# Performance work log

Hardware: AMD Instinct MI355X
Metric: run time of the kernel (lower is better)

Reference implementation:

```python
import jax, jax.numpy as jnp
import numpy as np
import math

BASE_RES = 16; SCALE = 1.47; N_LEVELS = 16; FDIM = 2; MAX_SPLASH = 4
LOG2 = 17; HM = 1 << LOG2; SPLITS = [0.9375, 0.875]  # sorted descending as in module


def _build_cfg():
    res = [int(BASE_RES * SCALE ** i) for i in range(N_LEVELS)]
    ns = [0] * N_LEVELS
    for i in range(N_LEVELS):
        for j, s in enumerate(SPLITS):
            if i >= N_LEVELS * s:
                ns[i] = MAX_SPLASH // (2 ** j)
                break
    nidx = [min(r ** 3, HM) for r in res]
    nfeat = [nidx[i] * max(ns[i], 1) for i in range(N_LEVELS)]
    ngau = [nidx[i] * ns[i] for i in range(N_LEVELS)]
    fb = np.concatenate([[0], np.cumsum(nfeat)]).astype(np.int64)
    gb = np.concatenate([[0], np.cumsum(ngau)]).astype(np.int64)
    return res, ns, nidx, fb, gb

RES, NS, NIDX, FB, GB = _build_cfg()
OFFS = np.array([[(k >> 2) & 1, (k >> 1) & 1, k & 1] for k in range(8)], dtype=np.int32)
PRIMES = np.array([1, 2654435761, 805459861], dtype=np.uint32)
SQRT2PI = math.sqrt(2.0 * math.pi)


def _corners_coeffs(coords, res):
    # coords: (N,3) in [0,1). Returns corners (N,8,3) int32 and trilinear coeffs (N,8).
    x = jnp.clip(res * coords, 0.0, res - 1.001)
    pos = jnp.floor(x).astype(jnp.int32)
    xf = x - pos.astype(coords.dtype)
    offs = jnp.asarray(OFFS)
    corners = pos[:, None, :] + offs[None]
    w = jnp.where(offs[None].astype(bool), xf[:, None, :], 1.0 - xf[:, None, :])
    return corners, jnp.prod(w, axis=-1)


def _hash_index(corners, res):
    # linear index if grid fits in table, else xor-prime spatial hash (mod 2^17)
    if res ** 3 <= HM:
        return corners[..., 0] + corners[..., 1] * res + corners[..., 2] * (res * res)
    c = corners.astype(jnp.uint32)
    p = jnp.asarray(PRIMES)
    h = (c[..., 0] * p[0]) ^ (c[..., 1] * p[1]) ^ (c[..., 2] * p[2])
    return (h & jnp.uint32(HM - 1)).astype(jnp.int32)


def setup_inputs() -> dict:
    key = jax.random.key(0)
    k1, k2, k3, k4 = jax.random.split(key, 4)
    N = 262144
    coords = jax.random.uniform(k1, (N, 3), dtype=jnp.float32)
    feats = 0.01 * jax.random.normal(k2, (int(FB[-1]), FDIM), dtype=jnp.float32)
    # means: uniform in a ball of radius 0.25 centered at 0.5 (init_mean)
    G = int(GB[-1])
    pts = jax.random.normal(k3, (G, 3), dtype=jnp.float32)
    r = jnp.sqrt(jax.random.uniform(jax.random.fold_in(k3, 1), (G, 1), dtype=jnp.float32))
    means = pts / jnp.linalg.norm(pts, axis=1, keepdims=True) * r * 0.25 + 0.5
    # stds: N(0.125, 0.02) as in fixed_std=False branch
    stds = 0.125 + 0.02 * jax.random.normal(k4, (G, 1), dtype=jnp.float32)
    return {"coords": coords, "feats": feats, "means": means, "stds": stds}


def reference(coords, feats, means, stds):
    out_feats = []
    out_gmm = []
    for i in range(N_LEVELS):
        res = RES[i]; ns = NS[i]
        corners, coeffs = _corners_coeffs(coords, res)  # (N,8,3), (N,8)
        idx = _hash_index(corners, res)                 # (N,8)
        f = feats[int(FB[i]):int(FB[i + 1])].reshape(-1, max(ns, 1), FDIM)[idx]  # (N,8,S,F)
        if ns:
            m = means[int(GB[i]):int(GB[i + 1])].reshape(-1, ns, 3)[idx]   # (N,8,S,3)
            s = jnp.abs(stds[int(GB[i]):int(GB[i + 1])].reshape(-1, ns, 1)[idx])  # (N,8,S,1)
            diff = coords[:, None, None, :] - m
            sq = jnp.sum(diff * diff / (2.0 * s * s + 1e-7), axis=-1, keepdims=True)
            gw = jnp.exp(-sq) / (SQRT2PI * s + 1e-7)                        # Gaussian weights
            dw = jnp.sum(jnp.abs(diff / s) ** 2, axis=-1, keepdims=True)    # normalized sq dist
            out_feats.append(jnp.einsum('nc,ncsf->nf', coeffs, gw * f))
            out_gmm.append(jnp.einsum('nc,ncs->n', coeffs, (gw * dw)[..., 0]))
        else:
            out_feats.append(jnp.einsum('nc,ncf->nf', coeffs, f[:, :, 0, :]))
    return jnp.concatenate(out_feats, axis=-1), jnp.stack(out_gmm, axis=-1)
```

## Files before the change

kernel.cpp:

```cpp
#include <hip/hip_runtime.h>
#include <math.h>


#define HMASK 131071
typedef float vf4 __attribute__((ext_vector_type(4)));
typedef float vf2 __attribute__((ext_vector_type(2)));
typedef _Float16 h8 __attribute__((ext_vector_type(8)));
typedef unsigned short u16;
typedef unsigned int u32;

#define LIN_OFF 2621440
#define L14_OFF 3670016
#define L15_OFF 7864320

__constant__ int c_fbh[10] = {180567,311639,442711,573783,704855,835927,
                              966999,1098071,1229143,1360215};
__constant__ int c_lres[4] = {16,23,34,50};
__constant__ int c_lfb[4]  = {0,4096,16263,55567};
__constant__ int c_h0res[4] = {74,109,161,237};
__constant__ int c_p1resA[3] = {348,512,753};
__constant__ int c_p1resB[3] = {1108,1629,2394};

__device__ __forceinline__ void corner_setup(int res, float cx, float cy, float cz,
                                             int& px, int& py, int& pz,
                                             float& fx, float& fy, float& fz)
{
    const float hi = (float)res - 1.001f;
    float x = fminf(fmaxf((float)res * cx, 0.0f), hi);
    float y = fminf(fmaxf((float)res * cy, 0.0f), hi);
    float z = fminf(fmaxf((float)res * cz, 0.0f), hi);
    px = (int)x; py = (int)y; pz = (int)z;
    fx = x - (float)px; fy = y - (float)py; fz = z - (float)pz;
}


__device__ __forceinline__ float2 linear_eval4(
    int res, int fbase, float cx, float cy, float cz,
    const float* __restrict__ feats)
{
    int px, py, pz; float fx, fy, fz;
    corner_setup(res, cx, cy, cz, px, py, pz, fx, fy, fz);
    int idxs[4]; float wyz[4];
#pragma unroll
    for (int j = 0; j < 4; ++j) {
        const int oy = (j >> 1) & 1, oz = j & 1;
        idxs[j] = px + (py + oy) * res + (pz + oz) * res * res;
        wyz[j] = (oy ? fy : 1.0f - fy) * (oz ? fz : 1.0f - fz);
    }
    vf4 fv[4];
#pragma unroll
    for (int j = 0; j < 4; ++j)
        fv[j] = *(const vf4*)(feats + (size_t)(fbase + idxs[j]) * 2);
    float a0 = 0.0f, a1 = 0.0f;
    const float gx = 1.0f - fx;
#pragma unroll
    for (int j = 0; j < 4; ++j) {
        a0 += wyz[j] * (gx * fv[j].x + fx * fv[j].z);
        a1 += wyz[j] * (gx * fv[j].y + fx * fv[j].w);
    }
    return make_float2(a0, a1);
}

__device__ __forceinline__ float2 plain_eval_f32h(
    int res, int fbase, float cx, float cy, float cz,
    const float* __restrict__ feats)
{
    int px, py, pz; float fx, fy, fz;
    corner_setup(res, cx, cy, cz, px, py, pz, fx, fy, fz);
    int   idxs[8];
    float ws[8];
#pragma unroll
    for (int k = 0; k < 8; ++k) {
        const int ox = (k >> 2) & 1, oy = (k >> 1) & 1, oz = k & 1;
        const int ix = px + ox, iy = py + oy, iz = pz + oz;
        ws[k] = (ox ? fx : 1.0f - fx) * (oy ? fy : 1.0f - fy) * (oz ? fz : 1.0f - fz);
        unsigned h = (unsigned)ix ^ ((unsigned)iy * 2654435761u) ^ ((unsigned)iz * 805459861u);
        idxs[k] = (int)(h & HMASK);
    }
    float2 fv[8];
#pragma unroll
    for (int k = 0; k < 8; ++k)
        fv[k] = *(const float2*)(feats + (size_t)(fbase + idxs[k]) * 2);
    float a0 = 0.0f, a1 = 0.0f;
#pragma unroll
    for (int k = 0; k < 8; ++k) { a0 += ws[k] * fv[k].x; a1 += ws[k] * fv[k].y; }
    return make_float2(a0, a1);
}


__device__ __forceinline__ float2 linear_eval4_fp8(
    int res, int ebase, float cx, float cy, float cz,
    const u32* __restrict__ ltab)
{
    int px, py, pz; float fx, fy, fz;
    corner_setup(res, cx, cy, cz, px, py, pz, fx, fy, fz);
    int idxs[4]; float wyz[4];
#pragma unroll
    for (int j = 0; j < 4; ++j) {
        const int oy = (j >> 1) & 1, oz = j & 1;
        idxs[j] = px + (py + oy) * res + (pz + oz) * res * res;
        wyz[j] = (oy ? fy : 1.0f - fy) * (oz ? fz : 1.0f - fz);
    }
    u32 u[4];
#pragma unroll
    for (int j = 0; j < 4; ++j) u[j] = ltab[ebase + idxs[j]];
    float a0 = 0.0f, a1 = 0.0f;
    const float gx = 1.0f - fx;
#pragma unroll
    for (int j = 0; j < 4; ++j) {
        vf2 lo = __builtin_amdgcn_cvt_pk_f32_fp8((int)u[j], false);
        vf2 hi = __builtin_amdgcn_cvt_pk_f32_fp8((int)u[j], true);
        a0 += wyz[j] * (gx * lo.x + fx * hi.x);
        a1 += wyz[j] * (gx * lo.y + fx * hi.y);
    }
    return make_float2(a0 * 0.0625f, a1 * 0.0625f);
}

__device__ __forceinline__ float2 plain_eval_fp8(
    int res, const u16* __restrict__ tab, float cx, float cy, float cz)
{
    int px, py, pz; float fx, fy, fz;
    corner_setup(res, cx, cy, cz, px, py, pz, fx, fy, fz);
    int   idxs[8];
    float ws[8];
#pragma unroll
    for (int k = 0; k < 8; ++k) {
        const int ox = (k >> 2) & 1, oy = (k >> 1) & 1, oz = k & 1;
        const int ix = px + ox, iy = py + oy, iz = pz + oz;
        ws[k] = (ox ? fx : 1.0f - fx) * (oy ? fy : 1.0f - fy) * (oz ? fz : 1.0f - fz);
        unsigned h = (unsigned)ix ^ ((unsigned)iy * 2654435761u) ^ ((unsigned)iz * 805459861u);
        idxs[k] = (int)(h & HMASK);
    }
    u16 v[8];
#pragma unroll
    for (int k = 0; k < 8; ++k) v[k] = tab[idxs[k]];
    float a0 = 0.0f, a1 = 0.0f;
#pragma unroll
    for (int k = 0; k < 8; ++k) {
        vf2 d = __builtin_amdgcn_cvt_pk_f32_fp8((int)v[k], false);
        a0 += ws[k] * d.x; a1 += ws[k] * d.y;
    }
    return make_float2(a0 * 0.0625f, a1 * 0.0625f);
}


__device__ __forceinline__ void gauss_pre(float w, float dx, float dy, float dz,
                                          float i2s, float inrm, float is2,
                                          float f0, float f1,
                                          float& a0, float& a1, float& ag)
{
    const float d2 = dx*dx + dy*dy + dz*dz;
    const float sq = d2 * i2s;
    const float gw = __expf(-sq) * inrm;
    const float wg = w * gw;
    a0 += wg * f0;
    a1 += wg * f1;
    ag += wg * (d2 * is2);
}

__device__ __forceinline__ void splash14_part(
    int k0, float cx, float cy, float cz, float cox, float coy, float coz,
    const h8* __restrict__ slots, float& a0, float& a1, float& ag)
{
    int px, py, pz; float fx, fy, fz;
    corner_setup(3520, cx, cy, cz, px, py, pz, fx, fy, fz);
    a0 = 0.0f; a1 = 0.0f; ag = 0.0f;
#pragma unroll
    for (int kk = 0; kk < 2; ++kk) {
        const int k = k0 + kk;
        const int ox = (k >> 2) & 1, oy = (k >> 1) & 1, oz = k & 1;
        const int ix = px + ox, iy = py + oy, iz = pz + oz;
        const float w = (ox ? fx : 1.0f - fx) * (oy ? fy : 1.0f - fy) * (oz ? fz : 1.0f - fz);
        unsigned h = (unsigned)ix ^ ((unsigned)iy * 2654435761u) ^ ((unsigned)iz * 805459861u);
        const int idx = (int)(h & HMASK);
        const h8* sp = slots + (size_t)idx * 2;
        h8 A = sp[0], B = sp[1];
        gauss_pre(w, cox - (float)A[0], coy - (float)A[1], coz - (float)A[2],
                  (float)A[6], (float)B[0], (float)B[2], (float)B[4], (float)B[5], a0, a1, ag);
        gauss_pre(w, cox - (float)A[3], coy - (float)A[4], coz - (float)A[5],
                  (float)A[7], (float)B[1], (float)B[3], (float)B[6], (float)B[7], a0, a1, ag);
    }
}

__device__ __forceinline__ void splash15_part(
    int k, float cx, float cy, float cz, float cox, float coy, float coz,
    const h8* __restrict__ slots, float& a0, float& a1, float& ag)
{
    int px, py, pz; float fx, fy, fz;
    corner_setup(5174, cx, cy, cz, px, py, pz, fx, fy, fz);
    a0 = 0.0f; a1 = 0.0f; ag = 0.0f;
    const int ox = (k >> 2) & 1, oy = (k >> 1) & 1, oz = k & 1;
    const int ix = px + ox, iy = py + oy, iz = pz + oz;
    const float w = (ox ? fx : 1.0f - fx) * (oy ? fy : 1.0f - fy) * (oz ? fz : 1.0f - fz);
    unsigned h = (unsigned)ix ^ ((unsigned)iy * 2654435761u) ^ ((unsigned)iz * 805459861u);
    const int idx = (int)(h & HMASK);
    const h8* sp = slots + (size_t)idx * 4;
    h8 A = sp[0], B = sp[1], C = sp[2], D = sp[3];
    gauss_pre(w, cox - (float)A[0], coy - (float)A[1], coz - (float)A[2],
              (float)B[4], (float)C[0], (float)C[4], (float)D[0], (float)D[1], a0, a1, ag);
    gauss_pre(w, cox - (float)A[3], coy - (float)A[4], coz - (float)A[5],
              (float)B[5], (float)C[1], (float)C[5], (float)D[2], (float)D[3], a0, a1, ag);
    gauss_pre(w, cox - (float)A[6], coy - (float)A[7], coz - (float)B[0],
              (float)B[6], (float)C[2], (float)C[6], (float)D[4], (float)D[5], a0, a1, ag);
    gauss_pre(w, cox - (float)B[1], coy - (float)B[2], coz - (float)B[3],
              (float)B[7], (float)C[3], (float)C[7], (float)D[6], (float)D[7], a0, a1, ag);
}

template<int NS, int KN>
__device__ __forceinline__ void splash_direct_part(
    int k0, int res, int fbase, int gbase, float cx, float cy, float cz,
    const float* __restrict__ feats, const float* __restrict__ means,
    const float* __restrict__ stds, float& a0, float& a1, float& ag)
{
    int px, py, pz; float fx, fy, fz;
    corner_setup(res, cx, cy, cz, px, py, pz, fx, fy, fz);
    a0 = 0.0f; a1 = 0.0f; ag = 0.0f;
#pragma unroll
    for (int kk = 0; kk < KN; ++kk) {
        const int k = k0 + kk;
        const int ox = (k >> 2) & 1, oy = (k >> 1) & 1, oz = k & 1;
        const int ix = px + ox, iy = py + oy, iz = pz + oz;
        const float w = (ox ? fx : 1.0f - fx) * (oy ? fy : 1.0f - fy) * (oz ? fz : 1.0f - fz);
        unsigned h = (unsigned)ix ^ ((unsigned)iy * 2654435761u) ^ ((unsigned)iz * 805459861u);
        const int idx = (int)(h & HMASK);
        const int grow = gbase + idx * NS;
        const float* m = means + (size_t)grow * 3;
        const float* s = stds + grow;
        const float* f = feats + (size_t)(fbase + idx * NS) * 2;
#pragma unroll
        for (int si = 0; si < NS; ++si) {
            const float dx = cx - m[3*si], dy = cy - m[3*si+1], dz = cz - m[3*si+2];
            const float sva = fabsf(s[si]);
            const float d2 = dx*dx + dy*dy + dz*dz;
            const float s2 = sva * sva;
            const float sq = d2 / (2.0f * s2 + 1e-7f);
            const float gw = expf(-sq) / (2.5066282746310002f * sva + 1e-7f);
            const float wg = w * gw;
            a0 += wg * f[2*si];
            a1 += wg * f[2*si+1];
            ag += wg * (d2 / s2);
        }
    }
}

__global__ __launch_bounds__(256) void repack_kernel(
    const float* __restrict__ means, const float* __restrict__ stds,
    const float* __restrict__ feats, unsigned char* __restrict__ wsb)
{
    const int b = blockIdx.x;
    const int tid = threadIdx.x;
    if (b < 640) {
        const int j   = b * 256 + tid;
        const int lvl = j >> 14;
        const int e8  = (j & 16383) * 8;
        const float* src = feats + (size_t)(c_fbh[lvl] + e8) * 2;
        uint4 u;
        u32* up = (u32*)&u;
#pragma unroll
        for (int p = 0; p < 4; ++p) {
            vf4 f = *(const vf4*)(src + 4 * p);
            int w = __builtin_amdgcn_cvt_pk_fp8_f32(16.0f * f.x, 16.0f * f.y, 0, false);
            w = __builtin_amdgcn_cvt_pk_fp8_f32(16.0f * f.z, 16.0f * f.w, w, true);
            up[p] = (u32)w;
        }
        *(uint4*)(wsb + (size_t)lvl * 262144 + (size_t)e8 * 2) = u;
    } else if (b < 1346) {
        const int e = (b - 640) * 256 + tid;
        if (e < 180567) {
            const float2 fa = *(const float2*)(feats + 2 * (size_t)e);
            const float2 fb = *(const float2*)(feats + 2 * (size_t)e + 2);
            int w = __builtin_amdgcn_cvt_pk_fp8_f32(16.0f * fa.x, 16.0f * fa.y, 0, false);
            w = __builtin_amdgcn_cvt_pk_fp8_f32(16.0f * fb.x, 16.0f * fb.y, w, true);
            ((u32*)(wsb + LIN_OFF))[e] = (u32)w;
        }
    } else if (b < 1858) {
        const int e = (b - 1346) * 256 + tid;
        const float2* m2 = (const float2*)(means + (size_t)e * 6);
        const float2 ma = m2[0], mb = m2[1], mc = m2[2];
        const float2 sv = *(const float2*)(stds + 2 * e);
        const float2* f2 = (const float2*)(feats + (size_t)(1491287 + 2 * e) * 2);
        const float2 fa = f2[0], fb = f2[1];
        const float s0 = fabsf(sv.x), s1 = fabsf(sv.y);
        h8 A, B;
        A[0] = (_Float16)(ma.x - 0.5f); A[1] = (_Float16)(ma.y - 0.5f); A[2] = (_Float16)(mb.x - 0.5f);
        A[3] = (_Float16)(mb.y - 0.5f); A[4] = (_Float16)(mc.x - 0.5f); A[5] = (_Float16)(mc.y - 0.5f);
        A[6] = (_Float16)(1.0f / (2.0f * s0 * s0 + 1e-7f));
        A[7] = (_Float16)(1.0f / (2.0f * s1 * s1 + 1e-7f));
        B[0] = (_Float16)(1.0f / (2.5066282746310002f * s0 + 1e-7f));
        B[1] = (_Float16)(1.0f / (2.5066282746310002f * s1 + 1e-7f));
        B[2] = (_Float16)(1.0f / (s0 * s0));
        B[3] = (_Float16)(1.0f / (s1 * s1));
        B[4] = (_Float16)fa.x; B[5] = (_Float16)fa.y; B[6] = (_Float16)fb.x; B[7] = (_Float16)fb.y;
        h8* dst = (h8*)(wsb + L14_OFF) + (size_t)e * 2;
        dst[0] = A; dst[1] = B;
    } else {
        const int e = (b - 1858) * 256 + tid;
        const vf4* m4 = (const vf4*)(means + (size_t)(262144 + 4 * e) * 3);
        const vf4 u = m4[0], v = m4[1], w = m4[2];
        const vf4 s4 = *(const vf4*)(stds + 262144 + 4 * e);
        const float2* f2 = (const float2*)(feats + (size_t)(1753431 + 4 * e) * 2);
        const float2 fa = f2[0], fb = f2[1], fc = f2[2], fd = f2[3];
        h8 A, B, C, D;
        A[0] = (_Float16)(u.x - 0.5f); A[1] = (_Float16)(u.y - 0.5f); A[2] = (_Float16)(u.z - 0.5f);
        A[3] = (_Float16)(u.w - 0.5f); A[4] = (_Float16)(v.x - 0.5f); A[5] = (_Float16)(v.y - 0.5f);
        A[6] = (_Float16)(v.z - 0.5f); A[7] = (_Float16)(v.w - 0.5f);
        B[0] = (_Float16)(w.x - 0.5f); B[1] = (_Float16)(w.y - 0.5f);
        B[2] = (_Float16)(w.z - 0.5f); B[3] = (_Float16)(w.w - 0.5f);
        const float sv[4] = {fabsf(s4.x), fabsf(s4.y), fabsf(s4.z), fabsf(s4.w)};
#pragma unroll
        for (int t = 0; t < 4; ++t) {
            B[4 + t] = (_Float16)(1.0f / (2.0f * sv[t] * sv[t] + 1e-7f));
            C[t]     = (_Float16)(1.0f / (2.5066282746310002f * sv[t] + 1e-7f));
            C[4 + t] = (_Float16)(1.0f / (sv[t] * sv[t]));
        }
        D[0] = (_Float16)fa.x; D[1] = (_Float16)fa.y; D[2] = (_Float16)fb.x; D[3] = (_Float16)fb.y;
        D[4] = (_Float16)fc.x; D[5] = (_Float16)fc.y; D[6] = (_Float16)fd.x; D[7] = (_Float16)fd.y;
        h8* dst = (h8*)(wsb + L15_OFF) + (size_t)e * 4;
        dst[0] = A; dst[1] = B; dst[2] = C; dst[3] = D;
    }
}

template<bool PACKED>
__global__ __launch_bounds__(256) void splash_enc(
    const float* __restrict__ coords, const float* __restrict__ feats,
    const float* __restrict__ means,  const float* __restrict__ stds,
    const unsigned char* __restrict__ wsb, float* __restrict__ out, int N)
{
    const int b = blockIdx.x;
    const int tid = threadIdx.x;
    const u16* ptab = (const u16*)wsb;
    const u32* ltab = (const u32*)(wsb + LIN_OFF);
    float* gmm = out + (size_t)N * 32;

    if (b < 4096) {
        const int t = b * 256 + tid;
        const int n = t >> 2, q = t & 3;
        const float cx = coords[3*n+0], cy = coords[3*n+1], cz = coords[3*n+2];
        float2 rlin, rhsh;
        if (PACKED) {
            rlin = linear_eval4_fp8(c_lres[q], c_lfb[q], cx, cy, cz, ltab);
            rhsh = plain_eval_fp8(c_h0res[q], ptab + q * 131072, cx, cy, cz);
        } else {
            rlin = linear_eval4(c_lres[q], c_lfb[q], cx, cy, cz, feats);
            rhsh = plain_eval_f32h(c_h0res[q], c_fbh[q], cx, cy, cz, feats);
        }
        *(float2*)(out + (size_t)n * 32 + 2 * q)     = rlin;
        *(float2*)(out + (size_t)n * 32 + 8 + 2 * q) = rhsh;
    } else if (b < 7168) {
        const int t = (b - 4096) * 256 + tid;
        const int n = (int)(((unsigned long long)(unsigned)t * 0xAAAAAAABull) >> 33);
        const int q = t - 3 * n;
        const float cx = coords[3*n+0], cy = coords[3*n+1], cz = coords[3*n+2];
        float2 rA, rB;
        if (PACKED) {
            rA = plain_eval_fp8(c_p1resA[q], ptab + (4 + q) * 131072, cx, cy, cz);
            rB = plain_eval_fp8(c_p1resB[q], ptab + (7 + q) * 131072, cx, cy, cz);
        } else {
            rA = plain_eval_f32h(c_p1resA[q], c_fbh[4 + q], cx, cy, cz, feats);
            rB = plain_eval_f32h(c_p1resB[q], c_fbh[7 + q], cx, cy, cz, feats);
        }
        *(float2*)(out + (size_t)n * 32 + 16 + 2 * q) = rA;
        *(float2*)(out + (size_t)n * 32 + 22 + 2 * q) = rB;
    } else if (b < 11264) {
        const int t = (b - 7168) * 256 + tid;
        const int n = t >> 2, q = t & 3;
        const float cx = coords[3*n+0], cy = coords[3*n+1], cz = coords[3*n+2];
        float a0, a1, ag;
        if (PACKED) {
            splash14_part(q * 2, cx, cy, cz, cx - 0.5f, cy - 0.5f, cz - 0.5f,
                          (const h8*)(wsb + L14_OFF), a0, a1, ag);
        } else {
            splash_direct_part<2,2>(q * 2, 3520, 1491287, 0, cx, cy, cz,
                                    feats, means, stds, a0, a1, ag);
        }
        a0 += __shfl_xor(a0, 1); a1 += __shfl_xor(a1, 1); ag += __shfl_xor(ag, 1);
        a0 += __shfl_xor(a0, 2); a1 += __shfl_xor(a1, 2); ag += __shfl_xor(ag, 2);
        if (q == 0) {
            *(float2*)(out + (size_t)n * 32 + 28) = make_float2(a0, a1);
            gmm[2 * n] = ag;
        }
    } else {
        const int t = (b - 11264) * 256 + tid;
        const int n = t >> 3, q = t & 7;
        const float cx = coords[3*n+0], cy = coords[3*n+1], cz = coords[3*n+2];
        float a0, a1, ag;
        if (PACKED) {
            splash15_part(q, cx, cy, cz, cx - 0.5f, cy - 0.5f, cz - 0.5f,
                          (const h8*)(wsb + L15_OFF), a0, a1, ag);
        } else {
            splash_direct_part<4,1>(q, 5174, 1753431, 262144, cx, cy, cz,
                                    feats, means, stds, a0, a1, ag);
        }
        a0 += __shfl_xor(a0, 1); a1 += __shfl_xor(a1, 1); ag += __shfl_xor(ag, 1);
        a0 += __shfl_xor(a0, 2); a1 += __shfl_xor(a1, 2); ag += __shfl_xor(ag, 2);
        a0 += __shfl_xor(a0, 4); a1 += __shfl_xor(a1, 4); ag += __shfl_xor(ag, 4);
        if (q == 0) {
            *(float2*)(out + (size_t)n * 32 + 30) = make_float2(a0, a1);
            gmm[2 * n + 1] = ag;
        }
    }
}

extern "C" void kernel_launch(void* const* d_in, const int* in_sizes, int n_in,
                              void* d_out, int out_size, void* d_ws, size_t ws_size,
                              hipStream_t stream) {
    const float* coords = (const float*)d_in[0];
    const float* feats  = (const float*)d_in[1];
    const float* means  = (const float*)d_in[2];
    const float* stds   = (const float*)d_in[3];
    float* out = (float*)d_out;
    const int N = in_sizes[0] / 3;

    const bool packed = (ws_size >= 17825792);
    if (packed) {
        repack_kernel<<<2370, 256, 0, stream>>>(means, stds, feats, (unsigned char*)d_ws);
        splash_enc<true><<<19456, 256, 0, stream>>>(coords, feats, means, stds,
                                                    (const unsigned char*)d_ws, out, N);
    } else {
        splash_enc<false><<<19456, 256, 0, stream>>>(coords, feats, means, stds,
                                                     (const unsigned char*)d_ws, out, N);
    }
}
```

Measured before the change: 215.2 us.

## Repack splash Gaussian slots per-Gaussian and split lanes by Gaussian instead of corner

The packed tables for levels 14 and 15 are re-laid out so that each 16-byte h8 holds one whole Gaussian (mean, inverse terms, features) rather than fields striped across several vectors. The eval kernels now give each lane one Gaussian slot across 4 corners (corner parity plus Gaussian index), so each lane does one 16-byte load per corner instead of loading the full 32- or 64-byte slot. The aim is to spread memory requests evenly across lanes and cut register pressure. In exchange, each lane now computes the hash and trilinear weight for four corners, which adds redundant ALU work.

```diff
diff --git a/kernel.cpp b/kernel.cpp
--- a/kernel.cpp
+++ b/kernel.cpp
@@ -158,52 +158,28 @@
     ag += wg * (d2 * is2);
 }
 
-__device__ __forceinline__ void splash14_part(
-    int k0, float cx, float cy, float cz, float cox, float coy, float coz,
-    const h8* __restrict__ slots, float& a0, float& a1, float& ag)
-{
-    int px, py, pz; float fx, fy, fz;
-    corner_setup(3520, cx, cy, cz, px, py, pz, fx, fy, fz);
+template<int NS>
+__device__ __forceinline__ void splash_quarters(
+    int res, const h8* __restrict__ quart, int g, int ch,
+    float cx, float cy, float cz, float cox, float coy, float coz,
+    float& a0, float& a1, float& ag)
+{
+    int px, py, pz; float fx, fy, fz;
+    corner_setup(res, cx, cy, cz, px, py, pz, fx, fy, fz);
     a0 = 0.0f; a1 = 0.0f; ag = 0.0f;
 #pragma unroll
-    for (int kk = 0; kk < 2; ++kk) {
-        const int k = k0 + kk;
+    for (int j = 0; j < 4; ++j) {
+        const int k = ch + 2 * j;
         const int ox = (k >> 2) & 1, oy = (k >> 1) & 1, oz = k & 1;
         const int ix = px + ox, iy = py + oy, iz = pz + oz;
         const float w = (ox ? fx : 1.0f - fx) * (oy ? fy : 1.0f - fy) * (oz ? fz : 1.0f - fz);
         unsigned h = (unsigned)ix ^ ((unsigned)iy * 2654435761u) ^ ((unsigned)iz * 805459861u);
         const int idx = (int)(h & HMASK);
-        const h8* sp = slots + (size_t)idx * 2;
-        h8 A = sp[0], B = sp[1];
-        gauss_pre(w, cox - (float)A[0], coy - (float)A[1], coz - (float)A[2],
-                  (float)A[6], (float)B[0], (float)B[2], (float)B[4], (float)B[5], a0, a1, ag);
-        gauss_pre(w, cox - (float)A[3], coy - (float)A[4], coz - (float)A[5],
-                  (float)A[7], (float)B[1], (float)B[3], (float)B[6], (float)B[7], a0, a1, ag);
-    }
-}
-
-__device__ __forceinline__ void splash15_part(
-    int k, float cx, float cy, float cz, float cox, float coy, float coz,
-    const h8* __restrict__ slots, float& a0, float& a1, float& ag)
-{
-    int px, py, pz; float fx, fy, fz;
-    corner_setup(5174, cx, cy, cz, px, py, pz, fx, fy, fz);
-    a0 = 0.0f; a1 = 0.0f; ag = 0.0f;
-    const int ox = (k >> 2) & 1, oy = (k >> 1) & 1, oz = k & 1;
-    const int ix = px + ox, iy = py + oy, iz = pz + oz;
-    const float w = (ox ? fx : 1.0f - fx) * (oy ? fy : 1.0f - fy) * (oz ? fz : 1.0f - fz);
-    unsigned h = (unsigned)ix ^ ((unsigned)iy * 2654435761u) ^ ((unsigned)iz * 805459861u);
-    const int idx = (int)(h & HMASK);
-    const h8* sp = slots + (size_t)idx * 4;
-    h8 A = sp[0], B = sp[1], C = sp[2], D = sp[3];
-    gauss_pre(w, cox - (float)A[0], coy - (float)A[1], coz - (float)A[2],
-              (float)B[4], (float)C[0], (float)C[4], (float)D[0], (float)D[1], a0, a1, ag);
-    gauss_pre(w, cox - (float)A[3], coy - (float)A[4], coz - (float)A[5],
-              (float)B[5], (float)C[1], (float)C[5], (float)D[2], (float)D[3], a0, a1, ag);
-    gauss_pre(w, cox - (float)A[6], coy - (float)A[7], coz - (float)B[0],
-              (float)B[6], (float)C[2], (float)C[6], (float)D[4], (float)D[5], a0, a1, ag);
-    gauss_pre(w, cox - (float)B[1], coy - (float)B[2], coz - (float)B[3],
-              (float)B[7], (float)C[3], (float)C[7], (float)D[6], (float)D[7], a0, a1, ag);
+        h8 Q = quart[(size_t)idx * NS + g];
+        gauss_pre(w, cox - (float)Q[0], coy - (float)Q[1], coz - (float)Q[2],
+                  (float)Q[3], (float)Q[4], (float)Q[5], (float)Q[6], (float)Q[7],
+                  a0, a1, ag);
+    }
 }
 
 template<int NS, int KN>
@@ -281,42 +257,43 @@
         const float2* f2 = (const float2*)(feats + (size_t)(1491287 + 2 * e) * 2);
         const float2 fa = f2[0], fb = f2[1];
         const float s0 = fabsf(sv.x), s1 = fabsf(sv.y);
-        h8 A, B;
-        A[0] = (_Float16)(ma.x - 0.5f); A[1] = (_Float16)(ma.y - 0.5f); A[2] = (_Float16)(mb.x - 0.5f);
-        A[3] = (_Float16)(mb.y - 0.5f); A[4] = (_Float16)(mc.x - 0.5f); A[5] = (_Float16)(mc.y - 0.5f);
-        A[6] = (_Float16)(1.0f / (2.0f * s0 * s0 + 1e-7f));
-        A[7] = (_Float16)(1.0f / (2.0f * s1 * s1 + 1e-7f));
-        B[0] = (_Float16)(1.0f / (2.5066282746310002f * s0 + 1e-7f));
-        B[1] = (_Float16)(1.0f / (2.5066282746310002f * s1 + 1e-7f));
-        B[2] = (_Float16)(1.0f / (s0 * s0));
-        B[3] = (_Float16)(1.0f / (s1 * s1));
-        B[4] = (_Float16)fa.x; B[5] = (_Float16)fa.y; B[6] = (_Float16)fb.x; B[7] = (_Float16)fb.y;
+        h8 Q0, Q1;
+        Q0[0] = (_Float16)(ma.x - 0.5f); Q0[1] = (_Float16)(ma.y - 0.5f); Q0[2] = (_Float16)(mb.x - 0.5f);
+        Q0[3] = (_Float16)(1.0f / (2.0f * s0 * s0 + 1e-7f));
+        Q0[4] = (_Float16)(1.0f / (2.5066282746310002f * s0 + 1e-7f));
+        Q0[5] = (_Float16)(1.0f / (s0 * s0));
+        Q0[6] = (_Float16)fa.x; Q0[7] = (_Float16)fa.y;
+        Q1[0] = (_Float16)(mb.y - 0.5f); Q1[1] = (_Float16)(mc.x - 0.5f); Q1[2] = (_Float16)(mc.y - 0.5f);
+        Q1[3] = (_Float16)(1.0f / (2.0f * s1 * s1 + 1e-7f));
+        Q1[4] = (_Float16)(1.0f / (2.5066282746310002f * s1 + 1e-7f));
+        Q1[5] = (_Float16)(1.0f / (s1 * s1));
+        Q1[6] = (_Float16)fb.x; Q1[7] = (_Float16)fb.y;
         h8* dst = (h8*)(wsb + L14_OFF) + (size_t)e * 2;
-        dst[0] = A; dst[1] = B;
+        dst[0] = Q0; dst[1] = Q1;
     } else {
         const int e = (b - 1858) * 256 + tid;
         const vf4* m4 = (const vf4*)(means + (size_t)(262144 + 4 * e) * 3);
         const vf4 u = m4[0], v = m4[1], w = m4[2];
         const vf4 s4 = *(const vf4*)(stds + 262144 + 4 * e);
         const float2* f2 = (const float2*)(feats + (size_t)(1753431 + 4 * e) * 2);
-        const float2 fa = f2[0], fb = f2[1], fc = f2[2], fd = f2[3];
-        h8 A, B, C, D;
-        A[0] = (_Float16)(u.x - 0.5f); A[1] = (_Float16)(u.y - 0.5f); A[2] = (_Float16)(u.z - 0.5f);
-        A[3] = (_Float16)(u.w - 0.5f); A[4] = (_Float16)(v.x - 0.5f); A[5] = (_Float16)(v.y - 0.5f);
-        A[6] = (_Float16)(v.z - 0.5f); A[7] = (_Float16)(v.w - 0.5f);
-        B[0] = (_Float16)(w.x - 0.5f); B[1] = (_Float16)(w.y - 0.5f);
-        B[2] = (_Float16)(w.z - 0.5f); B[3] = (_Float16)(w.w - 0.5f);
+        const float2 fv[4] = {f2[0], f2[1], f2[2], f2[3]};
+        const float mx[4] = {u.x, u.w, v.z, w.y};
+        const float my[4] = {u.y, v.x, v.w, w.z};
+        const float mz[4] = {u.z, v.y, w.x, w.w};
         const float sv[4] = {fabsf(s4.x), fabsf(s4.y), fabsf(s4.z), fabsf(s4.w)};
-#pragma unroll
-        for (int t = 0; t < 4; ++t) {
-            B[4 + t] = (_Float16)(1.0f / (2.0f * sv[t] * sv[t] + 1e-7f));
-            C[t]     = (_Float16)(1.0f / (2.5066282746310002f * sv[t] + 1e-7f));
-            C[4 + t] = (_Float16)(1.0f / (sv[t] * sv[t]));
-        }
-        D[0] = (_Float16)fa.x; D[1] = (_Float16)fa.y; D[2] = (_Float16)fb.x; D[3] = (_Float16)fb.y;
-        D[4] = (_Float16)fc.x; D[5] = (_Float16)fc.y; D[6] = (_Float16)fd.x; D[7] = (_Float16)fd.y;
         h8* dst = (h8*)(wsb + L15_OFF) + (size_t)e * 4;
-        dst[0] = A; dst[1] = B; dst[2] = C; dst[3] = D;
+#pragma unroll
+        for (int g = 0; g < 4; ++g) {
+            h8 Q;
+            Q[0] = (_Float16)(mx[g] - 0.5f);
+            Q[1] = (_Float16)(my[g] - 0.5f);
+            Q[2] = (_Float16)(mz[g] - 0.5f);
+            Q[3] = (_Float16)(1.0f / (2.0f * sv[g] * sv[g] + 1e-7f));
+            Q[4] = (_Float16)(1.0f / (2.5066282746310002f * sv[g] + 1e-7f));
+            Q[5] = (_Float16)(1.0f / (sv[g] * sv[g]));
+            Q[6] = (_Float16)fv[g].x; Q[7] = (_Float16)fv[g].y;
+            dst[g] = Q;
+        }
     }
 }
 
@@ -367,8 +344,8 @@
         const float cx = coords[3*n+0], cy = coords[3*n+1], cz = coords[3*n+2];
         float a0, a1, ag;
         if (PACKED) {
-            splash14_part(q * 2, cx, cy, cz, cx - 0.5f, cy - 0.5f, cz - 0.5f,
-                          (const h8*)(wsb + L14_OFF), a0, a1, ag);
+            splash_quarters<2>(3520, (const h8*)(wsb + L14_OFF), q & 1, q >> 1,
+                               cx, cy, cz, cx - 0.5f, cy - 0.5f, cz - 0.5f, a0, a1, ag);
         } else {
             splash_direct_part<2,2>(q * 2, 3520, 1491287, 0, cx, cy, cz,
                                     feats, means, stds, a0, a1, ag);
@@ -385,8 +362,8 @@
         const float cx = coords[3*n+0], cy = coords[3*n+1], cz = coords[3*n+2];
         float a0, a1, ag;
         if (PACKED) {
-            splash15_part(q, cx, cy, cz, cx - 0.5f, cy - 0.5f, cz - 0.5f,
-                          (const h8*)(wsb + L15_OFF), a0, a1, ag);
+            splash_quarters<4>(5174, (const h8*)(wsb + L15_OFF), q & 3, q >> 2,
+                               cx, cy, cz, cx - 0.5f, cy - 0.5f, cz - 0.5f, a0, a1, ag);
         } else {
             splash_direct_part<4,1>(q, 5174, 1753431, 262144, cx, cy, cz,
                                     feats, means, stds, a0, a1, ag);
```

Result: no change. 216.8 us (+0.7%).
